# Performance work log

Hardware: AMD Instinct MI355X
Metric: run time of the kernel (lower is better)

The kernel has to match this reference:

```python
import jax, jax.numpy as jnp
import numpy as np

D_MODEL = 768
D_COND = 128
N_LAYERS = 6
D_STATE = 16
D_CONV = 4
EXPAND = 2
D_INNER = EXPAND * D_MODEL            # 1536
DT_RANK = (D_MODEL + 15) // 16        # 48
BATCH, SEQ = 2, 1024
EPS = 1e-5


def setup_inputs() -> dict:
    key = jax.random.key(0)
    ks = iter(jax.random.split(key, 24))
    rn = lambda shape, s=0.02: jax.random.normal(next(ks), shape, dtype=jnp.float32) * s
    inp = {}
    inp["x"] = jax.random.normal(next(ks), (BATCH, SEQ, D_MODEL), dtype=jnp.float32)
    inp["condition"] = jax.random.normal(next(ks), (BATCH, D_COND), dtype=jnp.float32)
    # per-layer Mamba params, stacked on leading layer dim
    inp["in_proj_w"] = rn((N_LAYERS, 2 * D_INNER, D_MODEL))
    inp["conv_w"] = rn((N_LAYERS, D_INNER, D_CONV), 0.1)
    inp["conv_b"] = jnp.zeros((N_LAYERS, D_INNER), jnp.float32)
    inp["x_proj_w"] = rn((N_LAYERS, DT_RANK + 2 * D_STATE, D_INNER))
    inp["dt_proj_w"] = rn((N_LAYERS, D_INNER, DT_RANK), 0.1)
    inp["dt_proj_b"] = jnp.full((N_LAYERS, D_INNER), -4.0, jnp.float32)  # softplus -> small dt
    inp["A_log"] = jnp.tile(jnp.log(jnp.arange(1, D_STATE + 1, dtype=jnp.float32))[None, None, :], (N_LAYERS, D_INNER, 1))
    inp["D_skip"] = jnp.ones((N_LAYERS, D_INNER), jnp.float32)
    inp["out_proj_w"] = rn((N_LAYERS, D_MODEL, D_INNER))
    # post-residual LayerNorm affine per layer
    inp["norm_w"] = jnp.ones((N_LAYERS, D_MODEL), jnp.float32)
    inp["norm_b"] = jnp.zeros((N_LAYERS, D_MODEL), jnp.float32)
    # AdaLN: condition -> (scale, shift)
    inp["adaln_w"] = rn((N_LAYERS, 2 * D_MODEL, D_COND))
    inp["adaln_b"] = jnp.zeros((N_LAYERS, 2 * D_MODEL), jnp.float32)
    inp["final_norm_w"] = jnp.ones((D_MODEL,), jnp.float32)
    inp["final_norm_b"] = jnp.zeros((D_MODEL,), jnp.float32)
    return inp


def _ln(h, w, b):
    mu = jnp.mean(h, -1, keepdims=True)
    var = jnp.mean(jnp.square(h - mu), -1, keepdims=True)
    return (h - mu) * jax.lax.rsqrt(var + EPS) * w + b


def _ln_noaffine(h):
    mu = jnp.mean(h, -1, keepdims=True)
    var = jnp.mean(jnp.square(h - mu), -1, keepdims=True)
    return (h - mu) * jax.lax.rsqrt(var + EPS)


def _mamba(x, in_w, cw, cb, xp_w, dtp_w, dtp_b, A_log, D_skip, out_w):
    b, l, _ = x.shape
    xz = jnp.einsum('bld,ed->ble', x, in_w)                 # [b,l,2*di]
    xc, z = jnp.split(xz, 2, axis=-1)
    # causal depthwise conv over time
    xc_t = jnp.transpose(xc, (0, 2, 1))                     # [b,di,l]
    xc_t = jax.lax.conv_general_dilated(
        xc_t, cw[:, None, :], window_strides=(1,), padding=[(D_CONV - 1, 0)],
        dimension_numbers=('NCH', 'OIH', 'NCH'), feature_group_count=D_INNER)
    xc = jnp.transpose(xc_t + cb[None, :, None], (0, 2, 1))  # [b,l,di]
    xc = jax.nn.silu(xc)
    dbc = jnp.einsum('bld,ed->ble', xc, xp_w)                # [b,l,dt_rank+2*ds]
    dt = dbc[..., :DT_RANK]
    Bm = dbc[..., DT_RANK:DT_RANK + D_STATE]                 # [b,l,ds]
    Cm = dbc[..., DT_RANK + D_STATE:]                        # [b,l,ds]
    dt = jax.nn.softplus(jnp.einsum('blr,dr->bld', dt, dtp_w) + dtp_b)  # [b,l,di]
    A = -jnp.exp(A_log)                                      # [di,ds]

    def step(h, ts):
        dt_t, B_t, C_t, x_t = ts                             # [b,di],[b,ds],[b,ds],[b,di]
        dA = jnp.exp(dt_t[:, :, None] * A)                   # [b,di,ds]
        h = dA * h + (dt_t * x_t)[:, :, None] * B_t[:, None, :]
        y = jnp.sum(h * C_t[:, None, :], axis=-1)            # [b,di]
        return h, y

    h0 = jnp.zeros((b, D_INNER, D_STATE), x.dtype)
    ts = (jnp.transpose(dt, (1, 0, 2)), jnp.transpose(Bm, (1, 0, 2)),
          jnp.transpose(Cm, (1, 0, 2)), jnp.transpose(xc, (1, 0, 2)))
    h_final, y = jax.lax.scan(step, h0, ts)
    y = jnp.transpose(y, (1, 0, 2)) + D_skip * xc            # [b,l,di]
    y = y * jax.nn.silu(z)
    out = jnp.einsum('bld,ed->ble', y, out_w)                # [b,l,dm]
    return out, h_final


def reference(x, condition, in_proj_w, conv_w, conv_b, x_proj_w, dt_proj_w, dt_proj_b,
              A_log, D_skip, out_proj_w, norm_w, norm_b, adaln_w, adaln_b,
              final_norm_w, final_norm_b):
    h = x
    states = []
    for i in range(N_LAYERS):
        residual = h
        m, st = _mamba(h, in_proj_w[i], conv_w[i], conv_b[i], x_proj_w[i],
                       dt_proj_w[i], dt_proj_b[i], A_log[i], D_skip[i], out_proj_w[i])
        h = _ln(residual + m, norm_w[i], norm_b[i])
        ss = condition @ adaln_w[i].T + adaln_b[i]            # [b,2*dm]
        scale, shift = jnp.split(ss, 2, axis=-1)
        h = _ln_noaffine(h) * (1.0 + scale[:, None, :]) + shift[:, None, :]
        states.append(st)
    h = _ln(h, final_norm_w, final_norm_b)
    return h, jnp.stack(states)
```

## Files before the change

### kernel.cpp

```cpp
#include <hip/hip_runtime.h>
#include <hip/hip_bf16.h>

#define NL 6
#define DM 768
#define DI 1536
#define DS 16
#define NRANK 48
#define DBC 80
#define BATCH 2
#define SEQ 1024
#define NTOK (BATCH*SEQ)
#define NCHUNK 64
#define CHLEN 16
#define XKS 8
#define XKC (DI/XKS)

typedef __attribute__((ext_vector_type(8))) short short8;
typedef __attribute__((ext_vector_type(4))) float f32x4;
typedef __attribute__((ext_vector_type(4))) unsigned short ushort4v;

__device__ inline unsigned short f2bf(float f) {
  union { float f; unsigned u; } x; x.f = f;
  unsigned r = x.u + 0x7FFF + ((x.u >> 16) & 1);
  return (unsigned short)(r >> 16);
}
__device__ inline float bf2f(unsigned short s) {
  union { unsigned u; float f; } x; x.u = ((unsigned)s) << 16;
  return x.f;
}

__device__ inline void gl_lds16(const unsigned short* g, unsigned short* l) {
  __builtin_amdgcn_global_load_lds(
      (const __attribute__((address_space(1))) unsigned int*)(g),
      (__attribute__((address_space(3))) unsigned int*)(l),
      16, 0, 0);
}

#define U_X   (NTOK * DM / 4)
#define U_INW (NL * 2 * DI * DM / 4)
#define U_OUW (NL * DM * DI / 4)
#define U_XPW (NL * DBC * DI / 4)
#define U_DTW (NL * DI * 64 / 4)
#define U_NA  (NL * DI * DS / 4)
#define U_DTA (NTOK * 64 / 4)
#define U_ADA (NL * BATCH * 2 * DM)
#define U_ALL (U_X + U_INW + U_OUW + U_XPW + U_DTW + U_NA + U_DTA + U_ADA)

__device__ inline void cvt4_store(const float* s, unsigned short* d, int i) {
  f32x4 v = ((const f32x4*)s)[i];
  union { ushort4v u4; __hip_bfloat162 h[2]; } u;
  float2 p;
  p.x = v[0]; p.y = v[1]; u.h[0] = __float22bfloat162_rn(p);
  p.x = v[2]; p.y = v[3]; u.h[1] = __float22bfloat162_rn(p);
  ((ushort4v*)d)[i] = u.u4;
}

__global__ __launch_bounds__(256) void setup_k(
    const float* __restrict__ x, const float* __restrict__ inw,
    const float* __restrict__ ouw, const float* __restrict__ xpw,
    const float* __restrict__ dtpw, const float* __restrict__ alog,
    const float* __restrict__ cond, const float* __restrict__ adaw,
    const float* __restrict__ adab,
    unsigned short* __restrict__ xb, unsigned short* __restrict__ inwb,
    unsigned short* __restrict__ ouwb, unsigned short* __restrict__ xpwb,
    unsigned short* __restrict__ dtwb, float* __restrict__ na,
    unsigned short* __restrict__ dtA, float* __restrict__ ss,
    float* __restrict__ hc) {
  for (int i = blockIdx.x * 256 + threadIdx.x; i < U_ALL; i += gridDim.x * 256) {
    int k = i;
    if (k < U_X) {
      f32x4 v = ((const f32x4*)x)[k];
      ((f32x4*)hc)[k] = v;
      union { ushort4v u4; __hip_bfloat162 h[2]; } u;
      float2 p;
      p.x = v[0]; p.y = v[1]; u.h[0] = __float22bfloat162_rn(p);
      p.x = v[2]; p.y = v[3]; u.h[1] = __float22bfloat162_rn(p);
      ((ushort4v*)xb)[k] = u.u4;
      continue;
    }
    k -= U_X;
    if (k < U_INW) { cvt4_store(inw, inwb, k); continue; }
    k -= U_INW;
    if (k < U_OUW) { cvt4_store(ouw, ouwb, k); continue; }
    k -= U_OUW;
    if (k < U_XPW) { cvt4_store(xpw, xpwb, k); continue; }
    k -= U_XPW;
    if (k < U_DTW) {
      int col4 = (k & 15) * 4;
      int row = k >> 4;
      ushort4v u4;
      if (col4 < NRANK) {
        const float* src = dtpw + (size_t)row * NRANK + col4;
        u4[0] = f2bf(src[0]); u4[1] = f2bf(src[1]);
        u4[2] = f2bf(src[2]); u4[3] = f2bf(src[3]);
      } else {
        u4 = (ushort4v){0, 0, 0, 0};
      }
      *(ushort4v*)&dtwb[(size_t)row * 64 + col4] = u4;
      continue;
    }
    k -= U_DTW;
    if (k < U_NA) {
      f32x4 v = ((const f32x4*)alog)[k];
      f32x4 r;
#pragma unroll
      for (int e = 0; e < 4; e++) r[e] = -__expf(v[e]);
      ((f32x4*)na)[k] = r;
      continue;
    }
    k -= U_NA;
    if (k < U_DTA) {
      ((ushort4v*)dtA)[k] = (ushort4v){0, 0, 0, 0};
      continue;
    }
    k -= U_DTA;
    {
      int e = k % (2 * DM);
      int b = (k / (2 * DM)) % BATCH;
      int l = k / (BATCH * 2 * DM);
      const float* c = cond + b * 128;
      const float* wp = adaw + ((size_t)l * (2 * DM) + e) * 128;
      float s = adab[l * (2 * DM) + e];
      for (int kk = 0; kk < 128; kk++) s = fmaf(c[kk], wp[kk], s);
      ss[k] = s;
    }
  }
}

__global__ __launch_bounds__(256) void bt128b_k(
    const unsigned short* __restrict__ A, int lda,
    const unsigned short* __restrict__ W, int ldw,
    unsigned short* __restrict__ C, int ldc,
    int K) {
  __shared__ __align__(16) unsigned short As[2][128 * 32];
  __shared__ __align__(16) unsigned short Ws[2][128 * 32];
  const int tid = threadIdx.x;
  const int bm = blockIdx.y * 128;
  const int bn = blockIdx.x * 128;
  const int lane = tid & 63;
  const int wv = tid >> 6;
  const int wm = (wv >> 1) * 64;
  const int wn = (wv & 1) * 64;
  const int fr = lane & 15;
  const int fs = lane >> 4;

  const int r0 = tid >> 2;
  const int s0 = (tid & 3) ^ (r0 & 3);

  const unsigned short* gA0 = A + (size_t)(bm + r0) * lda + s0 * 8;
  const unsigned short* gA1 = A + (size_t)(bm + r0 + 64) * lda + s0 * 8;
  const unsigned short* gW0 = W + (size_t)(bn + r0) * ldw + s0 * 8;
  const unsigned short* gW1 = W + (size_t)(bn + r0 + 64) * ldw + s0 * 8;

  f32x4 acc[4][4];
#pragma unroll
  for (int i = 0; i < 4; i++)
#pragma unroll
    for (int j = 0; j < 4; j++) acc[i][j] = (f32x4){0.f, 0.f, 0.f, 0.f};

  gl_lds16(gA0, &As[0][0] + tid * 8);
  gl_lds16(gA1, &As[0][2048] + tid * 8);
  gl_lds16(gW0, &Ws[0][0] + tid * 8);
  gl_lds16(gW1, &Ws[0][2048] + tid * 8);
  __syncthreads();

  const int nk = K >> 5;
  int buf = 0;
  for (int kk = 0; kk < nk; kk++) {
    if (kk + 1 < nk) {
      const int k0 = (kk + 1) * 32;
      gl_lds16(gA0 + k0, &As[buf ^ 1][0] + tid * 8);
      gl_lds16(gA1 + k0, &As[buf ^ 1][2048] + tid * 8);
      gl_lds16(gW0 + k0, &Ws[buf ^ 1][0] + tid * 8);
      gl_lds16(gW1 + k0, &Ws[buf ^ 1][2048] + tid * 8);
    }

    short8 af[4], bf[4];
#pragma unroll
    for (int i = 0; i < 4; i++) {
      int rowa = wm + i * 16 + fr;
      af[i] = *(const short8*)&As[buf][rowa * 32 + ((fs ^ (rowa & 3)) * 8)];
      int rowb = wn + i * 16 + fr;
      bf[i] = *(const short8*)&Ws[buf][rowb * 32 + ((fs ^ (rowb & 3)) * 8)];
    }
#pragma unroll
    for (int i = 0; i < 4; i++)
#pragma unroll
      for (int j = 0; j < 4; j++)
        acc[i][j] = __builtin_amdgcn_mfma_f32_16x16x32_bf16(af[i], bf[j], acc[i][j], 0, 0, 0);

    __syncthreads();
    buf ^= 1;
  }

#pragma unroll
  for (int i = 0; i < 4; i++) {
#pragma unroll
    for (int j = 0; j < 4; j++) {
#pragma unroll
      for (int r = 0; r < 4; r++) {
        int row = bm + wm + i * 16 + fs * 4 + r;
        int col = bn + wn + j * 16 + fr;
        C[(size_t)row * ldc + col] = f2bf(acc[i][j][r]);
      }
    }
  }
}

template<int EPI>
__global__ __launch_bounds__(256) void bt64_k(
    const unsigned short* __restrict__ A, int lda,
    const unsigned short* __restrict__ W, int ldw,
    void* __restrict__ Cv, int ldc,
    int K,
    const float* __restrict__ bias,
    const float* __restrict__ resid) {
  __shared__ __align__(16) unsigned short As[2][64 * 32];
  __shared__ __align__(16) unsigned short Ws[2][64 * 32];
  const int tid = threadIdx.x;
  const int bm = blockIdx.y * 64;
  const int bn = blockIdx.x * 64;
  const int lane = tid & 63;
  const int wv = tid >> 6;
  const int wm = (wv >> 1) * 32;
  const int wn = (wv & 1) * 32;
  const int fr = lane & 15;
  const int fs = lane >> 4;

  const int r0 = tid >> 2;
  const int s0 = (tid & 3) ^ (r0 & 3);

  const unsigned short* gA = A + (size_t)(bm + r0) * lda + s0 * 8;
  const unsigned short* gW = W + (size_t)(bn + r0) * ldw + s0 * 8;

  f32x4 acc[2][2];
#pragma unroll
  for (int i = 0; i < 2; i++)
#pragma unroll
    for (int j = 0; j < 2; j++) acc[i][j] = (f32x4){0.f, 0.f, 0.f, 0.f};

  gl_lds16(gA, &As[0][0] + tid * 8);
  gl_lds16(gW, &Ws[0][0] + tid * 8);
  __syncthreads();

  const int nk = K >> 5;
  int buf = 0;
  for (int kk = 0; kk < nk; kk++) {
    if (kk + 1 < nk) {
      const int k0 = (kk + 1) * 32;
      gl_lds16(gA + k0, &As[buf ^ 1][0] + tid * 8);
      gl_lds16(gW + k0, &Ws[buf ^ 1][0] + tid * 8);
    }

    short8 af[2], bf[2];
#pragma unroll
    for (int i = 0; i < 2; i++) {
      int rowa = wm + i * 16 + fr;
      af[i] = *(const short8*)&As[buf][rowa * 32 + ((fs ^ (rowa & 3)) * 8)];
      int rowb = wn + i * 16 + fr;
      bf[i] = *(const short8*)&Ws[buf][rowb * 32 + ((fs ^ (rowb & 3)) * 8)];
    }
#pragma unroll
    for (int i = 0; i < 2; i++)
#pragma unroll
      for (int j = 0; j < 2; j++)
        acc[i][j] = __builtin_amdgcn_mfma_f32_16x16x32_bf16(af[i], bf[j], acc[i][j], 0, 0, 0);

    __syncthreads();
    buf ^= 1;
  }

#pragma unroll
  for (int i = 0; i < 2; i++) {
#pragma unroll
    for (int j = 0; j < 2; j++) {
#pragma unroll
      for (int r = 0; r < 4; r++) {
        int row = bm + wm + i * 16 + fs * 4 + r;
        int col = bn + wn + j * 16 + fr;
        float v = acc[i][j][r];
        if (EPI == 1) {
          float xv = v + bias[col];
          float sp = (xv > 20.f) ? xv : log1pf(__expf(xv));
          ((unsigned short*)Cv)[(size_t)row * ldc + col] = f2bf(sp);
        }
        if (EPI == 2) {
          ((float*)Cv)[(size_t)row * ldc + col] = v + resid[(size_t)row * ldc + col];
        }
      }
    }
  }
}

__global__ __launch_bounds__(256) void xp_k(
    const unsigned short* __restrict__ A,
    const unsigned short* __restrict__ W,
    unsigned short* __restrict__ part) {
  __shared__ __align__(16) unsigned short As[64][40];
  __shared__ __align__(16) unsigned short Ws[80][40];
  const int tid = threadIdx.x;
  const int ks = blockIdx.x;
  const int bm = blockIdx.y * 64;
  const int lane = tid & 63;
  const int wv = tid >> 6;
  const int fr = lane & 15;
  const int fs = lane >> 4;
  const int fk = fs * 8;

  const int ar = tid >> 2;
  const int ac = (tid & 3) * 8;
  const int k0base = ks * XKC;

  const unsigned short* gA  = A + (size_t)(bm + ar) * DI + k0base + ac;
  const unsigned short* gW0 = W + (size_t)ar * DI + k0base + ac;
  const unsigned short* gW1 = W + (size_t)(64 + ar) * DI + k0base + ac;

  f32x4 acc[5];
#pragma unroll
  for (int n = 0; n < 5; n++) acc[n] = (f32x4){0.f, 0.f, 0.f, 0.f};

  short8 aA, w0A, w1A;
  aA = *(const short8*)(gA);
  w0A = *(const short8*)(gW0);
  if (tid < 64) w1A = *(const short8*)(gW1);

  const int nk = XKC / 32;
  for (int kk = 0; kk < nk; kk++) {
    __syncthreads();
    *(short8*)&As[ar][ac] = aA;
    *(short8*)&Ws[ar][ac] = w0A;
    if (tid < 64) *(short8*)&Ws[64 + ar][ac] = w1A;
    __syncthreads();

    if (kk + 1 < nk) {
      const int k0 = (kk + 1) * 32;
      aA = *(const short8*)(gA + k0);
      w0A = *(const short8*)(gW0 + k0);
      if (tid < 64) w1A = *(const short8*)(gW1 + k0);
    }

    short8 af = *(const short8*)&As[wv * 16 + fr][fk];
#pragma unroll
    for (int n = 0; n < 5; n++) {
      short8 bf = *(const short8*)&Ws[n * 16 + fr][fk];
      acc[n] = __builtin_amdgcn_mfma_f32_16x16x32_bf16(af, bf, acc[n], 0, 0, 0);
    }
  }

#pragma unroll
  for (int n = 0; n < 5; n++) {
#pragma unroll
    for (int r = 0; r < 4; r++) {
      int row = bm + wv * 16 + fs * 4 + r;
      part[((size_t)ks * NTOK + row) * DBC + n * 16 + fr] = f2bf(acc[n][r]);
    }
  }
}

__global__ __launch_bounds__(256) void xp_reduce_k(const unsigned short* __restrict__ part,
                                                   unsigned short* __restrict__ dtA,
                                                   unsigned short* __restrict__ bc) {
  int i = blockIdx.x * 256 + threadIdx.x;
  const ushort4v* p4 = (const ushort4v*)part;
  const int stride4 = NTOK * DBC / 4;
  float s0 = 0.f, s1 = 0.f, s2 = 0.f, s3 = 0.f;
#pragma unroll
  for (int ks = 0; ks < XKS; ks++) {
    ushort4v v = p4[(size_t)ks * stride4 + i];
    s0 += bf2f(v[0]); s1 += bf2f(v[1]); s2 += bf2f(v[2]); s3 += bf2f(v[3]);
  }
  ushort4v o;
  o[0] = f2bf(s0); o[1] = f2bf(s1); o[2] = f2bf(s2); o[3] = f2bf(s3);
  int c4 = (i * 4) % DBC;
  int m = (i * 4) / DBC;
  if (c4 < NRANK) {
    *(ushort4v*)&dtA[(size_t)m * 64 + c4] = o;
  } else {
    *(ushort4v*)&bc[(size_t)m * 32 + (c4 - NRANK)] = o;
  }
}

__global__ __launch_bounds__(256) void conv_silu_k(const unsigned short* __restrict__ xz,
                                                   const float* __restrict__ cw,
                                                   const float* __restrict__ cb,
                                                   unsigned short* __restrict__ xcb) {
  const int d0 = (blockIdx.x * 256 + threadIdx.x) * 2;
  const int l0 = blockIdx.y * 16;
  const int b = blockIdx.z;
  const size_t mbase = (size_t)b * SEQ;
  const float wa0 = cw[d0 * 4 + 0], wa1 = cw[d0 * 4 + 1];
  const float wa2 = cw[d0 * 4 + 2], wa3 = cw[d0 * 4 + 3];
  const float wb0 = cw[d0 * 4 + 4], wb1 = cw[d0 * 4 + 5];
  const float wb2 = cw[d0 * 4 + 6], wb3 = cw[d0 * 4 + 7];
  const float ba = cb[d0], bb = cb[d0 + 1];

  float a3 = 0.f, a2 = 0.f, a1 = 0.f, b3 = 0.f, b2 = 0.f, b1 = 0.f;
  if (l0 >= 3) { ushort2 u = *(const ushort2*)&xz[(mbase + l0 - 3) * (2 * DI) + d0]; a3 = bf2f(u.x); b3 = bf2f(u.y); }
  if (l0 >= 2) { ushort2 u = *(const ushort2*)&xz[(mbase + l0 - 2) * (2 * DI) + d0]; a2 = bf2f(u.x); b2 = bf2f(u.y); }
  if (l0 >= 1) { ushort2 u = *(const ushort2*)&xz[(mbase + l0 - 1) * (2 * DI) + d0]; a1 = bf2f(u.x); b1 = bf2f(u.y); }
#pragma unroll
  for (int t = 0; t < 16; t++) {
    const int l = l0 + t;
    ushort2 u = *(const ushort2*)&xz[(mbase + l) * (2 * DI) + d0];
    float ca = bf2f(u.x), cbv = bf2f(u.y);
    float sa = ba + wa0 * a3 + wa1 * a2 + wa2 * a1 + wa3 * ca;
    float sb = bb + wb0 * b3 + wb1 * b2 + wb2 * b1 + wb3 * cbv;
    float ra = sa / (1.f + __expf(-sa));
    float rb = sb / (1.f + __expf(-sb));
    ushort2 o; o.x = f2bf(ra); o.y = f2bf(rb);
    *(ushort2*)&xcb[(mbase + l) * DI + d0] = o;
    a3 = a2; a2 = a1; a1 = ca;
    b3 = b2; b2 = b1; b1 = cbv;
  }
}

__global__ __launch_bounds__(256) void scan1_k(const unsigned short* __restrict__ dt,
                                               const unsigned short* __restrict__ xc,
                                               const unsigned short* __restrict__ bc,
                                               const float* __restrict__ negA_l,
                                               unsigned int* __restrict__ ch_pk,
                                               unsigned int* __restrict__ yc_pk) {
  __shared__ float Bs[CHLEN][DS];
  __shared__ float Cs[CHLEN][DS];
  const int tid = threadIdx.x;
  const int j = blockIdx.x;
  const int cg = blockIdx.y;
  const int b = cg / 6;
  const int d = (cg % 6) * 256 + tid;
  const int c = b * DI + d;
  const int m0 = b * SEQ + j * CHLEN;

  for (int e = tid; e < CHLEN * 32; e += 256) {
    int row = e >> 5, col = e & 31;
    float v = bf2f(bc[(size_t)(m0 + row) * 32 + col]);
    if (col < DS) Bs[row][col] = v; else Cs[row][col - DS] = v;
  }

  float Av[DS];
  const float* na = negA_l + (size_t)d * DS;
#pragma unroll
  for (int s = 0; s < DS; s++) Av[s] = na[s];
  const float Av0 = Av[0];
  bool fast = true;
#pragma unroll
  for (int s = 0; s < DS; s++)
    fast = fast && (fabsf(Av[s] - (s + 1) * Av0) <= 1e-4f * (s + 1));

  float dts[CHLEN], xcs[CHLEN];
#pragma unroll
  for (int t = 0; t < CHLEN; t++) {
    dts[t] = bf2f(dt[(size_t)(m0 + t) * DI + d]);
    xcs[t] = bf2f(xc[(size_t)(m0 + t) * DI + d]);
  }
  __syncthreads();

  float h[DS];
#pragma unroll
  for (int s = 0; s < DS; s++) h[s] = 0.f;
  float cd = 0.f;

  for (int t = 0; t < CHLEN; t++) {
    float dtv = dts[t];
    cd += dtv;
    float dtx = dtv * xcs[t];
    float ysum = 0.f;
    if (fast) {
      float e1 = __expf(dtv * Av0);
      float dA = e1;
      h[0] = fmaf(dA, h[0], dtx * Bs[t][0]);
      ysum = fmaf(h[0], Cs[t][0], ysum);
#pragma unroll
      for (int s = 1; s < DS; s++) {
        dA *= e1;
        h[s] = fmaf(dA, h[s], dtx * Bs[t][s]);
        ysum = fmaf(h[s], Cs[t][s], ysum);
      }
    } else {
#pragma unroll
      for (int s = 0; s < DS; s++) {
        float dA = __expf(dtv * Av[s]);
        h[s] = fmaf(dA, h[s], dtx * Bs[t][s]);
        ysum = fmaf(h[s], Cs[t][s], ysum);
      }
    }
    yc_pk[(size_t)(m0 + t) * DI + d] =
        (unsigned int)f2bf(ysum) | ((unsigned int)f2bf(cd) << 16);
  }

  size_t base = ((size_t)j * (BATCH * DI) + c) * DS;
#pragma unroll
  for (int s = 0; s < DS; s++) {
    unsigned int pk = (unsigned int)f2bf(__expf(cd * Av[s]))
                    | ((unsigned int)f2bf(h[s]) << 16);
    ch_pk[base + s] = pk;
  }
}

__global__ __launch_bounds__(256) void scan2_k(const unsigned int* __restrict__ ch_pk,
                                               unsigned short* __restrict__ hin,
                                               float* __restrict__ states_out) {
  int idx = blockIdx.x * 256 + threadIdx.x;
  const int stride = BATCH * DI * DS;
  float h = 0.f;
  for (int j = 0; j < NCHUNK; j++) {
    hin[(size_t)j * stride + idx] = f2bf(h);
    unsigned int pk = ch_pk[(size_t)j * stride + idx];
    float ca = bf2f((unsigned short)(pk & 0xFFFF));
    float hl = bf2f((unsigned short)(pk >> 16));
    h = fmaf(ca, h, hl);
  }
  states_out[idx] = h;
}

__global__ __launch_bounds__(256) void scanfix_k(const unsigned int* __restrict__ yc_pk,
                                                 const unsigned short* __restrict__ xc,
                                                 const unsigned short* __restrict__ xz,
                                                 const unsigned short* __restrict__ bc,
                                                 const float* __restrict__ negA_l,
                                                 const float* __restrict__ Dsk,
                                                 const unsigned short* __restrict__ hin,
                                                 unsigned short* __restrict__ y) {
  int idx = blockIdx.x * 256 + threadIdx.x;
  int d = idx % DI;
  int m = idx / DI;
  int b = m / SEQ;
  int j = (m % SEQ) / CHLEN;
  unsigned int pk = yc_pk[idx];
  float yv = bf2f((unsigned short)(pk & 0xFFFF));
  float cd = bf2f((unsigned short)(pk >> 16));
  const f32x4* na4 = (const f32x4*)(negA_l + (size_t)d * DS);
  const ushort4v* cp4 = (const ushort4v*)(bc + (size_t)m * 32 + DS);
  const ushort4v* h4 = (const ushort4v*)(hin + ((size_t)j * (BATCH * DI) + (size_t)b * DI + d) * DS);
  float corr = 0.f;
#pragma unroll
  for (int q = 0; q < 4; q++) {
    f32x4 na = na4[q];
    ushort4v cp = cp4[q];
    ushort4v hh = h4[q];
#pragma unroll
    for (int e = 0; e < 4; e++)
      corr = fmaf(__expf(cd * na[e]) * bf2f(hh[e]), bf2f(cp[e]), corr);
  }
  yv += corr;
  float xv = bf2f(xc[idx]);
  float zv = bf2f(xz[(size_t)m * (2 * DI) + DI + d]);
  float sig = 1.f / (1.f + __expf(-zv));
  y[idx] = f2bf((yv + Dsk[d] * xv) * (zv * sig));
}

template<bool ADA>
__global__ __launch_bounds__(256) void ln_k(const float* __restrict__ in,
                                            const float* __restrict__ w,
                                            const float* __restrict__ bb,
                                            const float* __restrict__ ss,
                                            float* __restrict__ out,
                                            unsigned short* __restrict__ outb) {
  __shared__ float red[8];
  const int row = blockIdx.x;
  const int bt = row / SEQ;
  const int tid = threadIdx.x;
  const float* x = in + (size_t)row * DM;
  float v[3];
#pragma unroll
  for (int i = 0; i < 3; i++) v[i] = x[tid + i * 256];
  float s1 = v[0] + v[1] + v[2];
  float s2 = v[0]*v[0] + v[1]*v[1] + v[2]*v[2];
#pragma unroll
  for (int o = 32; o > 0; o >>= 1) { s1 += __shfl_down(s1, o); s2 += __shfl_down(s2, o); }
  int wv = tid >> 6, ln = tid & 63;
  if (ln == 0) { red[wv*2] = s1; red[wv*2+1] = s2; }
  __syncthreads();
  s1 = red[0] + red[2] + red[4] + red[6];
  s2 = red[1] + red[3] + red[5] + red[7];
  float mu = s1 * (1.f / DM);
  float var = s2 * (1.f / DM) - mu * mu;
  float rs = rsqrtf(var + 1e-5f);
  float t[3];
#pragma unroll
  for (int i = 0; i < 3; i++) {
    int c = tid + i * 256;
    t[i] = (v[i] - mu) * rs * w[c] + bb[c];
  }
  if (!ADA) {
#pragma unroll
    for (int i = 0; i < 3; i++) out[(size_t)row * DM + tid + i * 256] = t[i];
    return;
  }
  __syncthreads();
  s1 = t[0] + t[1] + t[2];
  s2 = t[0]*t[0] + t[1]*t[1] + t[2]*t[2];
#pragma unroll
  for (int o = 32; o > 0; o >>= 1) { s1 += __shfl_down(s1, o); s2 += __shfl_down(s2, o); }
  if (ln == 0) { red[wv*2] = s1; red[wv*2+1] = s2; }
  __syncthreads();
  s1 = red[0] + red[2] + red[4] + red[6];
  s2 = red[1] + red[3] + red[5] + red[7];
  float mu2 = s1 * (1.f / DM);
  float var2 = s2 * (1.f / DM) - mu2 * mu2;
  float rs2 = rsqrtf(var2 + 1e-5f);
#pragma unroll
  for (int i = 0; i < 3; i++) {
    int c = tid + i * 256;
    float sc = ss[bt * (2 * DM) + c];
    float sh = ss[bt * (2 * DM) + DM + c];
    float r = (t[i] - mu2) * rs2 * (1.f + sc) + sh;
    out[(size_t)row * DM + c] = r;
    outb[(size_t)row * DM + c] = f2bf(r);
  }
}

extern "C" void kernel_launch(void* const* d_in, const int* in_sizes, int n_in,
                              void* d_out, int out_size, void* d_ws, size_t ws_size,
                              hipStream_t stream) {
  const float* x      = (const float*)d_in[0];
  const float* cond   = (const float*)d_in[1];
  const float* in_w   = (const float*)d_in[2];
  const float* conv_w = (const float*)d_in[3];
  const float* conv_b = (const float*)d_in[4];
  const float* xp_w   = (const float*)d_in[5];
  const float* dtp_w  = (const float*)d_in[6];
  const float* dtp_b  = (const float*)d_in[7];
  const float* A_log  = (const float*)d_in[8];
  const float* Dsk    = (const float*)d_in[9];
  const float* out_w  = (const float*)d_in[10];
  const float* norm_w = (const float*)d_in[11];
  const float* norm_b = (const float*)d_in[12];
  const float* ada_w  = (const float*)d_in[13];
  const float* ada_b  = (const float*)d_in[14];
  const float* fn_w   = (const float*)d_in[15];
  const float* fn_b   = (const float*)d_in[16];

  float* out_h = (float*)d_out;
  float* out_states = out_h + (size_t)NTOK * DM;

  float* p = (float*)d_ws;
  float* h_cur = p; p += (size_t)NTOK * DM;
  float* res2  = p; p += (size_t)NTOK * DM;
  float* ss    = p; p += (size_t)NL * BATCH * 2 * DM;
  float* negA  = p; p += (size_t)NL * DI * DS;
  unsigned int* ch_pk = (unsigned int*)p; p += (size_t)NCHUNK * BATCH * DI * DS;
  unsigned int* yc_pk = (unsigned int*)p; p += (size_t)NTOK * DI;
  unsigned short* q = (unsigned short*)p;
  unsigned short* hin      = q; q += (size_t)NCHUNK * BATCH * DI * DS;
  unsigned short* in_w_bf  = q; q += (size_t)NL * 2 * DI * DM;
  unsigned short* out_w_bf = q; q += (size_t)NL * DM * DI;
  unsigned short* xp_w_bf  = q; q += (size_t)NL * DBC * DI;
  unsigned short* dtw_bf   = q; q += (size_t)NL * DI * 64;
  unsigned short* h_bf     = q; q += (size_t)NTOK * DM;
  unsigned short* xz_bf    = q; q += (size_t)NTOK * 2 * DI;
  unsigned short* xc_bf    = q; q += (size_t)NTOK * DI;
  unsigned short* dtb_bf   = q; q += (size_t)NTOK * DI;
  unsigned short* yb_bf    = q; q += (size_t)NTOK * DI;
  unsigned short* part_bf  = q; q += (size_t)XKS * NTOK * DBC;
  unsigned short* dtA_bf   = q; q += (size_t)NTOK * 64;
  unsigned short* bc_bf    = q; q += (size_t)NTOK * 32;

  setup_k<<<2048, 256, 0, stream>>>(x, in_w, out_w, xp_w, dtp_w, A_log,
                                    cond, ada_w, ada_b,
                                    h_bf, in_w_bf, out_w_bf, xp_w_bf, dtw_bf,
                                    negA, dtA_bf, ss, h_cur);

  for (int l = 0; l < NL; l++) {
    bt128b_k<<<dim3(24, 16), 256, 0, stream>>>(
        h_bf, DM, in_w_bf + (size_t)l * 2 * DI * DM, DM, xz_bf, 2 * DI, DM);
    conv_silu_k<<<dim3(DI / 512, SEQ / 16, BATCH), 256, 0, stream>>>(
        xz_bf, conv_w + (size_t)l * DI * 4, conv_b + (size_t)l * DI, xc_bf);
    xp_k<<<dim3(XKS, NTOK / 64), 256, 0, stream>>>(
        xc_bf, xp_w_bf + (size_t)l * DBC * DI, part_bf);
    xp_reduce_k<<<NTOK * DBC / 4 / 256, 256, 0, stream>>>(part_bf, dtA_bf, bc_bf);
    bt64_k<1><<<dim3(DI / 64, NTOK / 64), 256, 0, stream>>>(
        dtA_bf, 64, dtw_bf + (size_t)l * DI * 64, 64, dtb_bf, DI,
        64, dtp_b + (size_t)l * DI, nullptr);
    scan1_k<<<dim3(NCHUNK, 12), 256, 0, stream>>>(
        dtb_bf, xc_bf, bc_bf, negA + (size_t)l * DI * DS, ch_pk, yc_pk);
    scan2_k<<<192, 256, 0, stream>>>(
        ch_pk, hin, out_states + (size_t)l * BATCH * DI * DS);
    scanfix_k<<<NTOK * DI / 256, 256, 0, stream>>>(
        yc_pk, xc_bf, xz_bf, bc_bf, negA + (size_t)l * DI * DS,
        Dsk + (size_t)l * DI, hin, yb_bf);
    bt64_k<2><<<dim3(DM / 64, NTOK / 64), 256, 0, stream>>>(
        yb_bf, DI, out_w_bf + (size_t)l * DM * DI, DI, res2, DM,
        DI, nullptr, h_cur);
    ln_k<true><<<NTOK, 256, 0, stream>>>(
        res2, norm_w + (size_t)l * DM, norm_b + (size_t)l * DM,
        ss + (size_t)l * BATCH * 2 * DM, h_cur, h_bf);
  }
  ln_k<false><<<NTOK, 256, 0, stream>>>(h_cur, fn_w, fn_b, nullptr, out_h, nullptr);
}
```

Measured before the change: 754.9 us.

## Triple-buffer GEMM LDS pipeline and split setup into conversion and AdaLN kernels

Both bf16 MFMA GEMM kernels move from double to triple LDS buffering, prefetching two K-steps ahead. They use explicit vmcnt waits and raw s_barrier in place of __syncthreads, so global loads overlap further with MFMA work. The setup kernel is split into a vectorised 8-wide conversion kernel and a separate AdaLN projection kernel. The fp32 copy of x into h_cur is removed by having layer 0's residual read x directly. Triple buffering raises LDS use per block, and the hand-counted vmcnt values must match the number of outstanding loads exactly.

```diff
diff --git a/kernel.cpp b/kernel.cpp
--- a/kernel.cpp
+++ b/kernel.cpp
@@ -16,6 +16,7 @@
 #define XKC (DI/XKS)
 
 typedef __attribute__((ext_vector_type(8))) short short8;
+typedef __attribute__((ext_vector_type(8))) unsigned short ushort8v;
 typedef __attribute__((ext_vector_type(4))) float f32x4;
 typedef __attribute__((ext_vector_type(4))) unsigned short ushort4v;
 
@@ -36,95 +37,92 @@
       16, 0, 0);
 }
 
-#define U_X   (NTOK * DM / 4)
-#define U_INW (NL * 2 * DI * DM / 4)
-#define U_OUW (NL * DM * DI / 4)
-#define U_XPW (NL * DBC * DI / 4)
-#define U_DTW (NL * DI * 64 / 4)
-#define U_NA  (NL * DI * DS / 4)
-#define U_DTA (NTOK * 64 / 4)
-#define U_ADA (NL * BATCH * 2 * DM)
-#define U_ALL (U_X + U_INW + U_OUW + U_XPW + U_DTW + U_NA + U_DTA + U_ADA)
-
-__device__ inline void cvt4_store(const float* s, unsigned short* d, int i) {
-  f32x4 v = ((const f32x4*)s)[i];
-  union { ushort4v u4; __hip_bfloat162 h[2]; } u;
+#define V_X   (NTOK * DM / 8)
+#define V_INW (NL * 2 * DI * DM / 8)
+#define V_OUW (NL * DM * DI / 8)
+#define V_XPW (NL * DBC * DI / 8)
+#define V_DTW (NL * DI * 64 / 8)
+#define V_NA  (NL * DI * DS / 8)
+#define V_DTA (NTOK * 64 / 8)
+#define V_ALL (V_X + V_INW + V_OUW + V_XPW + V_DTW + V_NA + V_DTA)
+
+__device__ inline ushort8v cvt8v(f32x4 a, f32x4 b) {
+  union { ushort8v u8; __hip_bfloat162 h[4]; } u;
   float2 p;
-  p.x = v[0]; p.y = v[1]; u.h[0] = __float22bfloat162_rn(p);
-  p.x = v[2]; p.y = v[3]; u.h[1] = __float22bfloat162_rn(p);
-  ((ushort4v*)d)[i] = u.u4;
-}
-
-__global__ __launch_bounds__(256) void setup_k(
+  p.x = a[0]; p.y = a[1]; u.h[0] = __float22bfloat162_rn(p);
+  p.x = a[2]; p.y = a[3]; u.h[1] = __float22bfloat162_rn(p);
+  p.x = b[0]; p.y = b[1]; u.h[2] = __float22bfloat162_rn(p);
+  p.x = b[2]; p.y = b[3]; u.h[3] = __float22bfloat162_rn(p);
+  return u.u8;
+}
+__device__ inline void cvt8_store(const float* s, unsigned short* d, int i) {
+  f32x4 a = ((const f32x4*)s)[i * 2];
+  f32x4 b = ((const f32x4*)s)[i * 2 + 1];
+  ((ushort8v*)d)[i] = cvt8v(a, b);
+}
+
+__global__ __launch_bounds__(256) void cvt_k(
     const float* __restrict__ x, const float* __restrict__ inw,
     const float* __restrict__ ouw, const float* __restrict__ xpw,
     const float* __restrict__ dtpw, const float* __restrict__ alog,
-    const float* __restrict__ cond, const float* __restrict__ adaw,
-    const float* __restrict__ adab,
     unsigned short* __restrict__ xb, unsigned short* __restrict__ inwb,
     unsigned short* __restrict__ ouwb, unsigned short* __restrict__ xpwb,
     unsigned short* __restrict__ dtwb, float* __restrict__ na,
-    unsigned short* __restrict__ dtA, float* __restrict__ ss,
-    float* __restrict__ hc) {
-  for (int i = blockIdx.x * 256 + threadIdx.x; i < U_ALL; i += gridDim.x * 256) {
+    unsigned short* __restrict__ dtA) {
+  for (int i = blockIdx.x * 256 + threadIdx.x; i < V_ALL; i += gridDim.x * 256) {
     int k = i;
-    if (k < U_X) {
-      f32x4 v = ((const f32x4*)x)[k];
-      ((f32x4*)hc)[k] = v;
-      union { ushort4v u4; __hip_bfloat162 h[2]; } u;
-      float2 p;
-      p.x = v[0]; p.y = v[1]; u.h[0] = __float22bfloat162_rn(p);
-      p.x = v[2]; p.y = v[3]; u.h[1] = __float22bfloat162_rn(p);
-      ((ushort4v*)xb)[k] = u.u4;
+    if (k < V_X) { cvt8_store(x, xb, k); continue; }
+    k -= V_X;
+    if (k < V_INW) { cvt8_store(inw, inwb, k); continue; }
+    k -= V_INW;
+    if (k < V_OUW) { cvt8_store(ouw, ouwb, k); continue; }
+    k -= V_OUW;
+    if (k < V_XPW) { cvt8_store(xpw, xpwb, k); continue; }
+    k -= V_XPW;
+    if (k < V_DTW) {
+      int col8 = (k & 7) * 8;
+      int row = k >> 3;
+      ushort8v u8;
+      if (col8 < NRANK) {
+        const float* src = dtpw + (size_t)row * NRANK + col8;
+        f32x4 a = *(const f32x4*)src;
+        f32x4 b = *(const f32x4*)(src + 4);
+        u8 = cvt8v(a, b);
+      } else {
+        u8 = (ushort8v){0,0,0,0,0,0,0,0};
+      }
+      *(ushort8v*)&dtwb[(size_t)row * 64 + col8] = u8;
       continue;
     }
-    k -= U_X;
-    if (k < U_INW) { cvt4_store(inw, inwb, k); continue; }
-    k -= U_INW;
-    if (k < U_OUW) { cvt4_store(ouw, ouwb, k); continue; }
-    k -= U_OUW;
-    if (k < U_XPW) { cvt4_store(xpw, xpwb, k); continue; }
-    k -= U_XPW;
-    if (k < U_DTW) {
-      int col4 = (k & 15) * 4;
-      int row = k >> 4;
-      ushort4v u4;
-      if (col4 < NRANK) {
-        const float* src = dtpw + (size_t)row * NRANK + col4;
-        u4[0] = f2bf(src[0]); u4[1] = f2bf(src[1]);
-        u4[2] = f2bf(src[2]); u4[3] = f2bf(src[3]);
-      } else {
-        u4 = (ushort4v){0, 0, 0, 0};
-      }
-      *(ushort4v*)&dtwb[(size_t)row * 64 + col4] = u4;
+    k -= V_DTW;
+    if (k < V_NA) {
+      f32x4 a = ((const f32x4*)alog)[k * 2];
+      f32x4 b = ((const f32x4*)alog)[k * 2 + 1];
+      f32x4 ra, rb;
+#pragma unroll
+      for (int e = 0; e < 4; e++) { ra[e] = -__expf(a[e]); rb[e] = -__expf(b[e]); }
+      ((f32x4*)na)[k * 2] = ra;
+      ((f32x4*)na)[k * 2 + 1] = rb;
       continue;
     }
-    k -= U_DTW;
-    if (k < U_NA) {
-      f32x4 v = ((const f32x4*)alog)[k];
-      f32x4 r;
-#pragma unroll
-      for (int e = 0; e < 4; e++) r[e] = -__expf(v[e]);
-      ((f32x4*)na)[k] = r;
-      continue;
-    }
-    k -= U_NA;
-    if (k < U_DTA) {
-      ((ushort4v*)dtA)[k] = (ushort4v){0, 0, 0, 0};
-      continue;
-    }
-    k -= U_DTA;
-    {
-      int e = k % (2 * DM);
-      int b = (k / (2 * DM)) % BATCH;
-      int l = k / (BATCH * 2 * DM);
-      const float* c = cond + b * 128;
-      const float* wp = adaw + ((size_t)l * (2 * DM) + e) * 128;
-      float s = adab[l * (2 * DM) + e];
-      for (int kk = 0; kk < 128; kk++) s = fmaf(c[kk], wp[kk], s);
-      ss[k] = s;
-    }
-  }
+    k -= V_NA;
+    ((ushort8v*)dtA)[k] = (ushort8v){0,0,0,0,0,0,0,0};
+  }
+}
+
+__global__ __launch_bounds__(256) void ada_k(const float* __restrict__ cond,
+                                             const float* __restrict__ aw,
+                                             const float* __restrict__ ab,
+                                             float* __restrict__ ss) {
+  int idx = blockIdx.x * 256 + threadIdx.x;
+  int e = idx % (2 * DM);
+  int b = (idx / (2 * DM)) % BATCH;
+  int l = idx / (BATCH * 2 * DM);
+  const float* c = cond + b * 128;
+  const float* wp = aw + ((size_t)l * (2 * DM) + e) * 128;
+  float s = ab[l * (2 * DM) + e];
+  for (int k = 0; k < 128; k++) s = fmaf(c[k], wp[k], s);
+  ss[idx] = s;
 }
 
 __global__ __launch_bounds__(256) void bt128b_k(
@@ -132,8 +130,8 @@
     const unsigned short* __restrict__ W, int ldw,
     unsigned short* __restrict__ C, int ldc,
     int K) {
-  __shared__ __align__(16) unsigned short As[2][128 * 32];
-  __shared__ __align__(16) unsigned short Ws[2][128 * 32];
+  __shared__ __align__(16) unsigned short As[3][128 * 32];
+  __shared__ __align__(16) unsigned short Ws[3][128 * 32];
   const int tid = threadIdx.x;
   const int bm = blockIdx.y * 128;
   const int bn = blockIdx.x * 128;
@@ -158,30 +156,42 @@
 #pragma unroll
     for (int j = 0; j < 4; j++) acc[i][j] = (f32x4){0.f, 0.f, 0.f, 0.f};
 
+  const int nk = K >> 5;
   gl_lds16(gA0, &As[0][0] + tid * 8);
   gl_lds16(gA1, &As[0][2048] + tid * 8);
   gl_lds16(gW0, &Ws[0][0] + tid * 8);
   gl_lds16(gW1, &Ws[0][2048] + tid * 8);
-  __syncthreads();
-
-  const int nk = K >> 5;
-  int buf = 0;
+  if (nk > 1) {
+    gl_lds16(gA0 + 32, &As[1][0] + tid * 8);
+    gl_lds16(gA1 + 32, &As[1][2048] + tid * 8);
+    gl_lds16(gW0 + 32, &Ws[1][0] + tid * 8);
+    gl_lds16(gW1 + 32, &Ws[1][2048] + tid * 8);
+  }
+
   for (int kk = 0; kk < nk; kk++) {
-    if (kk + 1 < nk) {
-      const int k0 = (kk + 1) * 32;
-      gl_lds16(gA0 + k0, &As[buf ^ 1][0] + tid * 8);
-      gl_lds16(gA1 + k0, &As[buf ^ 1][2048] + tid * 8);
-      gl_lds16(gW0 + k0, &Ws[buf ^ 1][0] + tid * 8);
-      gl_lds16(gW1 + k0, &Ws[buf ^ 1][2048] + tid * 8);
-    }
+    const int b = kk % 3;
+    if (kk + 2 < nk) {
+      const int k0 = (kk + 2) * 32;
+      const int nb = (kk + 2) % 3;
+      gl_lds16(gA0 + k0, &As[nb][0] + tid * 8);
+      gl_lds16(gA1 + k0, &As[nb][2048] + tid * 8);
+      gl_lds16(gW0 + k0, &Ws[nb][0] + tid * 8);
+      gl_lds16(gW1 + k0, &Ws[nb][2048] + tid * 8);
+    }
+    const int ahead = (nk - 1 - kk >= 2) ? 2 : (nk - 1 - kk);
+    if (ahead == 2)      asm volatile("s_waitcnt vmcnt(8)" : : : "memory");
+    else if (ahead == 1) asm volatile("s_waitcnt vmcnt(4)" : : : "memory");
+    else                 asm volatile("s_waitcnt vmcnt(0)" : : : "memory");
+    __builtin_amdgcn_s_barrier();
+    __builtin_amdgcn_sched_barrier(0);
 
     short8 af[4], bf[4];
 #pragma unroll
     for (int i = 0; i < 4; i++) {
       int rowa = wm + i * 16 + fr;
-      af[i] = *(const short8*)&As[buf][rowa * 32 + ((fs ^ (rowa & 3)) * 8)];
+      af[i] = *(const short8*)&As[b][rowa * 32 + ((fs ^ (rowa & 3)) * 8)];
       int rowb = wn + i * 16 + fr;
-      bf[i] = *(const short8*)&Ws[buf][rowb * 32 + ((fs ^ (rowb & 3)) * 8)];
+      bf[i] = *(const short8*)&Ws[b][rowb * 32 + ((fs ^ (rowb & 3)) * 8)];
     }
 #pragma unroll
     for (int i = 0; i < 4; i++)
@@ -189,8 +199,7 @@
       for (int j = 0; j < 4; j++)
         acc[i][j] = __builtin_amdgcn_mfma_f32_16x16x32_bf16(af[i], bf[j], acc[i][j], 0, 0, 0);
 
-    __syncthreads();
-    buf ^= 1;
+    __builtin_amdgcn_s_barrier();
   }
 
 #pragma unroll
@@ -215,8 +224,8 @@
     int K,
     const float* __restrict__ bias,
     const float* __restrict__ resid) {
-  __shared__ __align__(16) unsigned short As[2][64 * 32];
-  __shared__ __align__(16) unsigned short Ws[2][64 * 32];
+  __shared__ __align__(16) unsigned short As[3][64 * 32];
+  __shared__ __align__(16) unsigned short Ws[3][64 * 32];
   const int tid = threadIdx.x;
   const int bm = blockIdx.y * 64;
   const int bn = blockIdx.x * 64;
@@ -239,26 +248,36 @@
 #pragma unroll
     for (int j = 0; j < 2; j++) acc[i][j] = (f32x4){0.f, 0.f, 0.f, 0.f};
 
+  const int nk = K >> 5;
   gl_lds16(gA, &As[0][0] + tid * 8);
   gl_lds16(gW, &Ws[0][0] + tid * 8);
-  __syncthreads();
-
-  const int nk = K >> 5;
-  int buf = 0;
+  if (nk > 1) {
+    gl_lds16(gA + 32, &As[1][0] + tid * 8);
+    gl_lds16(gW + 32, &Ws[1][0] + tid * 8);
+  }
+
   for (int kk = 0; kk < nk; kk++) {
-    if (kk + 1 < nk) {
-      const int k0 = (kk + 1) * 32;
-      gl_lds16(gA + k0, &As[buf ^ 1][0] + tid * 8);
-      gl_lds16(gW + k0, &Ws[buf ^ 1][0] + tid * 8);
-    }
+    const int b = kk % 3;
+    if (kk + 2 < nk) {
+      const int k0 = (kk + 2) * 32;
+      const int nb = (kk + 2) % 3;
+      gl_lds16(gA + k0, &As[nb][0] + tid * 8);
+      gl_lds16(gW + k0, &Ws[nb][0] + tid * 8);
+    }
+    const int ahead = (nk - 1 - kk >= 2) ? 2 : (nk - 1 - kk);
+    if (ahead == 2)      asm volatile("s_waitcnt vmcnt(4)" : : : "memory");
+    else if (ahead == 1) asm volatile("s_waitcnt vmcnt(2)" : : : "memory");
+    else                 asm volatile("s_waitcnt vmcnt(0)" : : : "memory");
+    __builtin_amdgcn_s_barrier();
+    __builtin_amdgcn_sched_barrier(0);
 
     short8 af[2], bf[2];
 #pragma unroll
     for (int i = 0; i < 2; i++) {
       int rowa = wm + i * 16 + fr;
-      af[i] = *(const short8*)&As[buf][rowa * 32 + ((fs ^ (rowa & 3)) * 8)];
+      af[i] = *(const short8*)&As[b][rowa * 32 + ((fs ^ (rowa & 3)) * 8)];
       int rowb = wn + i * 16 + fr;
-      bf[i] = *(const short8*)&Ws[buf][rowb * 32 + ((fs ^ (rowb & 3)) * 8)];
+      bf[i] = *(const short8*)&Ws[b][rowb * 32 + ((fs ^ (rowb & 3)) * 8)];
     }
 #pragma unroll
     for (int i = 0; i < 2; i++)
@@ -266,8 +285,7 @@
       for (int j = 0; j < 2; j++)
         acc[i][j] = __builtin_amdgcn_mfma_f32_16x16x32_bf16(af[i], bf[j], acc[i][j], 0, 0, 0);
 
-    __syncthreads();
-    buf ^= 1;
+    __builtin_amdgcn_s_barrier();
   }
 
 #pragma unroll
@@ -655,10 +673,10 @@
   unsigned short* dtA_bf   = q; q += (size_t)NTOK * 64;
   unsigned short* bc_bf    = q; q += (size_t)NTOK * 32;
 
-  setup_k<<<2048, 256, 0, stream>>>(x, in_w, out_w, xp_w, dtp_w, A_log,
-                                    cond, ada_w, ada_b,
-                                    h_bf, in_w_bf, out_w_bf, xp_w_bf, dtw_bf,
-                                    negA, dtA_bf, ss, h_cur);
+  cvt_k<<<2048, 256, 0, stream>>>(x, in_w, out_w, xp_w, dtp_w, A_log,
+                                  h_bf, in_w_bf, out_w_bf, xp_w_bf, dtw_bf,
+                                  negA, dtA_bf);
+  ada_k<<<72, 256, 0, stream>>>(cond, ada_w, ada_b, ss);
 
   for (int l = 0; l < NL; l++) {
     bt128b_k<<<dim3(24, 16), 256, 0, stream>>>(
@@ -680,7 +698,7 @@
         Dsk + (size_t)l * DI, hin, yb_bf);
     bt64_k<2><<<dim3(DM / 64, NTOK / 64), 256, 0, stream>>>(
         yb_bf, DI, out_w_bf + (size_t)l * DM * DI, DI, res2, DM,
-        DI, nullptr, h_cur);
+        DI, nullptr, (l == 0) ? x : h_cur);
     ln_k<true><<<NTOK, 256, 0, stream>>>(
         res2, norm_w + (size_t)l * DM, norm_b + (size_t)l * DM,
         ss + (size_t)l * BATCH * 2 * DM, h_cur, h_bf);
```

Result: no change. 747.2 us (-1.0%).
